# Optimization experiments

Measured on AMD Instinct MI355X. Metric: run time of the kernel, lower is better.

Reference implementation:

```python
import jax, jax.numpy as jnp
import numpy as np

B = 8192
IN = 2048
H = 2048


def setup_inputs() -> dict:
    key = jax.random.key(0)
    ks = jax.random.split(key, 7)
    s_in = 1.0 / np.sqrt(IN)
    s_h = 1.0 / np.sqrt(H)
    inp = jax.random.normal(ks[0], (B, IN), jnp.float32)
    h0 = jax.random.normal(ks[1], (B, H), jnp.float32)
    c0 = jax.random.normal(ks[2], (B, H), jnp.float32)
    # Packed gate weights: columns ordered [i, f, o, g], each block size H.
    # Equivalent to the 8 separate nn.Linear layers (i_w,f_w,o_w,g_w / i_u,f_u,o_u,g_u).
    W = jax.random.uniform(ks[3], (IN, 4 * H), jnp.float32, -s_in, s_in)
    b_w = jax.random.uniform(ks[4], (4 * H,), jnp.float32, -s_in, s_in)
    U = jax.random.uniform(ks[5], (H, 4 * H), jnp.float32, -s_h, s_h)
    b_u = jax.random.uniform(ks[6], (4 * H,), jnp.float32, -s_h, s_h)
    return {"inp": inp, "h0": h0, "c0": c0, "W": W, "b_w": b_w, "U": U, "b_u": b_u}


def reference(inp, h0, c0, W, b_w, U, b_u):
    # Two big GEMMs instead of eight small ones; identical math.
    gates = inp @ W + b_w + h0 @ U + b_u  # [B, 4H]
    i_g, f_g, o_g, g_g = jnp.split(gates, 4, axis=-1)
    i = jax.nn.sigmoid(i_g)
    f = jax.nn.sigmoid(f_g)
    o = jax.nn.sigmoid(o_g)
    g = jnp.tanh(g_g)
    c = f * c0 + i * g
    h = o * jnp.tanh(c)
    return (h, c)
```

## Files before the change

### kernel.cpp

```cpp
#include <hip/hip_runtime.h>
#include <hip/hip_bf16.h>

#define B_DIM 8192
#define IN_DIM 2048
#define H_DIM 2048
#define K_DIM 4096
#define N4H   8192
#define NT    64

using short8 = __attribute__((ext_vector_type(8))) short;
using f32x4  = __attribute__((ext_vector_type(4))) float;
using u16x4  = __attribute__((ext_vector_type(4))) unsigned short;

__device__ __forceinline__ unsigned short f2bf(float f) {
  union { float f; unsigned int u; } v; v.f = f;
  unsigned int u = v.u;
  return (unsigned short)((u + 0x7FFFu + ((u >> 16) & 1u)) >> 16);
}

__global__ __launch_bounds__(256) void pack_a(const float* __restrict__ inp,
                                              const float* __restrict__ h0,
                                              unsigned short* __restrict__ Ap) {
  size_t idx = ((size_t)blockIdx.x * 256 + threadIdx.x) * 4;
  int b = (int)(idx >> 12);
  int k = (int)(idx & 4095);
  const float* src = (k < IN_DIM) ? (inp + (size_t)b * IN_DIM + k)
                                  : (h0  + (size_t)b * H_DIM + (k - IN_DIM));
  float4 v = *(const float4*)src;
  u16x4 o = { f2bf(v.x), f2bf(v.y), f2bf(v.z), f2bf(v.w) };
  *(u16x4*)&Ap[idx] = o;
}

__global__ __launch_bounds__(256) void pack_b(const float* __restrict__ W,
                                              const float* __restrict__ U,
                                              unsigned short* __restrict__ Bp) {
  __shared__ float tile[64][17];
  const int c0 = blockIdx.x * 16;
  const int k0 = blockIdx.y * 64;
  const int gate  = (c0 >> 4) & 3;
  const int jbase = (c0 >> 6) * 16;
  const int colbase = gate * 2048 + jbase;
  const int t  = threadIdx.x;
  const int cc = t & 15;
  const int r0 = t >> 4;
#pragma unroll
  for (int rr = 0; rr < 4; ++rr) {
    int k = k0 + r0 + rr * 16;
    const float* src = (k < IN_DIM) ? (W + (size_t)k * N4H)
                                    : (U + (size_t)(k - IN_DIM) * N4H);
    tile[r0 + rr * 16][cc] = src[colbase + cc];
  }
  __syncthreads();
  const int c   = t >> 4;
  const int kk0 = (t & 15) * 4;
  u16x4 o = { f2bf(tile[kk0 + 0][c]), f2bf(tile[kk0 + 1][c]),
              f2bf(tile[kk0 + 2][c]), f2bf(tile[kk0 + 3][c]) };
  *(u16x4*)&Bp[(size_t)(c0 + c) * K_DIM + k0 + kk0] = o;
}

__global__ __launch_bounds__(512, 2) void lstm_gemm(
    const unsigned short* __restrict__ Ap,
    const unsigned short* __restrict__ Bp,
    const float* __restrict__ c0,
    const float* __restrict__ b_w,
    const float* __restrict__ b_u,
    float* __restrict__ out) {
  __shared__ unsigned short lds[65536];

  const int t     = threadIdx.x;
  const int lane  = t & 63;
  const int wid   = t >> 6;
  const int wr    = wid >> 2;
  const int wc    = wid & 3;
  const int laneM = lane & 15;
  const int laneG = lane >> 4;

  const int wg  = blockIdx.x;
  const int swz = (wg & 7) * 128 + (wg >> 3);
  const int bm  = swz >> 5;
  const int bn  = swz & 31;

  const int rt   = t >> 3;
  const int gt   = t & 7;
  const int gsw  = gt ^ (rt & 7);
  const unsigned short* gA = Ap + (size_t)(bm * 256 + rt) * K_DIM + gsw * 8;
  const unsigned short* gB = Bp + (size_t)(bn * 256 + rt) * K_DIM + gsw * 8;

#define STAGE(gptr, ldsoff)                                                   \
  __builtin_amdgcn_global_load_lds(                                           \
      (const __attribute__((address_space(1))) void*)(gptr),                  \
      (__attribute__((address_space(3))) void*)&lds[(ldsoff) + t * 8], 16, 0, 0)

  const int sbit = laneM & 7;
  int aoff[2], boff[2];
#pragma unroll
  for (int kk = 0; kk < 2; ++kk) {
    aoff[kk] = wr * 8192 + laneM * 64 + ((kk * 4 + laneG) ^ sbit) * 8;
    boff[kk] = 16384 + (wc >> 1) * 8192 + ((wc & 1) * 64 + laneM) * 64
               + ((kk * 4 + laneG) ^ sbit) * 8;
  }

  f32x4 acc[8][4];
#pragma unroll
  for (int m = 0; m < 8; ++m)
#pragma unroll
    for (int n = 0; n < 4; ++n)
      acc[m][n] = (f32x4){0.f, 0.f, 0.f, 0.f};

  short8 bf[4][2];

  STAGE(gB,               16384 + 0);
  STAGE(gB +  64 * K_DIM, 16384 + 4096);
  STAGE(gB + 128 * K_DIM, 16384 + 8192);
  STAGE(gB + 192 * K_DIM, 16384 + 12288);
  STAGE(gA,               0);
  STAGE(gA +  64 * K_DIM, 4096);
  STAGE(gA + 128 * K_DIM, 8192);
  STAGE(gA + 192 * K_DIM, 12288);
  asm volatile("s_waitcnt vmcnt(0)" ::: "memory");
  __builtin_amdgcn_s_barrier();

  for (int kt = 0; kt < NT - 1; ++kt) {
    const int cb = (kt & 1) * 32768;
    const int db = ((kt & 1) ^ 1) * 32768;
    const unsigned short* gA1 = gA + (kt + 1) * 64;
    const unsigned short* gB1 = gB + (kt + 1) * 64;
#pragma unroll
    for (int q = 0; q < 4; ++q) {
      short8 af[2][2];
      if (q == 0) {
#pragma unroll
        for (int n = 0; n < 4; ++n)
#pragma unroll
          for (int kk = 0; kk < 2; ++kk)
            bf[n][kk] = *(const short8*)&lds[cb + boff[kk] + n * 1024];
      }
#pragma unroll
      for (int i = 0; i < 2; ++i)
#pragma unroll
        for (int kk = 0; kk < 2; ++kk)
          af[i][kk] = *(const short8*)&lds[cb + aoff[kk] + (2 * q + i) * 1024];

      if (q == 0) {
        STAGE(gB1,               db + 16384 + 0);
        STAGE(gB1 +  64 * K_DIM, db + 16384 + 4096);
      } else if (q == 1) {
        STAGE(gB1 + 128 * K_DIM, db + 16384 + 8192);
        STAGE(gB1 + 192 * K_DIM, db + 16384 + 12288);
        asm volatile("s_waitcnt vmcnt(4)" ::: "memory");
      } else if (q == 2) {
        STAGE(gA1,               db + 0);
        STAGE(gA1 + 128 * K_DIM, db + 8192);
      } else {
        STAGE(gA1 +  64 * K_DIM, db + 4096);
        STAGE(gA1 + 192 * K_DIM, db + 12288);
        asm volatile("s_waitcnt vmcnt(2)" ::: "memory");
      }
      __builtin_amdgcn_s_barrier();
      __builtin_amdgcn_s_setprio(1);
#pragma unroll
      for (int i = 0; i < 2; ++i)
#pragma unroll
        for (int n = 0; n < 4; ++n)
#pragma unroll
          for (int kk = 0; kk < 2; ++kk)
            acc[2 * q + i][n] = __builtin_amdgcn_mfma_f32_16x16x32_bf16(
                af[i][kk], bf[n][kk], acc[2 * q + i][n], 0, 0, 0);
      __builtin_amdgcn_s_setprio(0);
      __builtin_amdgcn_s_barrier();
    }
  }

  asm volatile("s_waitcnt vmcnt(0)" ::: "memory");
  __builtin_amdgcn_s_barrier();
  {
    const int cb = ((NT - 1) & 1) * 32768;
#pragma unroll
    for (int q = 0; q < 4; ++q) {
      short8 af[2][2];
      if (q == 0) {
#pragma unroll
        for (int n = 0; n < 4; ++n)
#pragma unroll
          for (int kk = 0; kk < 2; ++kk)
            bf[n][kk] = *(const short8*)&lds[cb + boff[kk] + n * 1024];
      }
#pragma unroll
      for (int i = 0; i < 2; ++i)
#pragma unroll
        for (int kk = 0; kk < 2; ++kk)
          af[i][kk] = *(const short8*)&lds[cb + aoff[kk] + (2 * q + i) * 1024];
      __builtin_amdgcn_s_setprio(1);
#pragma unroll
      for (int i = 0; i < 2; ++i)
#pragma unroll
        for (int n = 0; n < 4; ++n)
#pragma unroll
          for (int kk = 0; kk < 2; ++kk)
            acc[2 * q + i][n] = __builtin_amdgcn_mfma_f32_16x16x32_bf16(
                af[i][kk], bf[n][kk], acc[2 * q + i][n], 0, 0, 0);
      __builtin_amdgcn_s_setprio(0);
    }
  }

  const int j = (bn * 4 + wc) * 16 + laneM;
  float bias[4];
#pragma unroll
  for (int g = 0; g < 4; ++g)
    bias[g] = b_w[g * 2048 + j] + b_u[g * 2048 + j];

  const int rbase = bm * 256 + wr * 128 + laneG * 4;
  float* outH = out;
  float* outC = out + (size_t)B_DIM * H_DIM;
#pragma unroll
  for (int m = 0; m < 8; ++m) {
#pragma unroll
    for (int r = 0; r < 4; ++r) {
      const int bi = rbase + m * 16 + r;
      const size_t off = (size_t)bi * H_DIM + j;
      float ig = acc[m][0][r] + bias[0];
      float fg = acc[m][1][r] + bias[1];
      float og = acc[m][2][r] + bias[2];
      float gg = acc[m][3][r] + bias[3];
      float iv = 1.f / (1.f + __expf(-ig));
      float fv = 1.f / (1.f + __expf(-fg));
      float ov = 1.f / (1.f + __expf(-og));
      float gv = 2.f / (1.f + __expf(-2.f * gg)) - 1.f;
      float cv = fv * c0[off] + iv * gv;
      float tc = 2.f / (1.f + __expf(-2.f * cv)) - 1.f;
      outH[off] = ov * tc;
      outC[off] = cv;
    }
  }
}

extern "C" void kernel_launch(void* const* d_in, const int* in_sizes, int n_in,
                              void* d_out, int out_size, void* d_ws, size_t ws_size,
                              hipStream_t stream) {
  const float* inp = (const float*)d_in[0];
  const float* h0  = (const float*)d_in[1];
  const float* c0  = (const float*)d_in[2];
  const float* W   = (const float*)d_in[3];
  const float* b_w = (const float*)d_in[4];
  const float* U   = (const float*)d_in[5];
  const float* b_u = (const float*)d_in[6];
  float* out = (float*)d_out;

  unsigned short* Ap = (unsigned short*)d_ws;
  unsigned short* Bp = Ap + (size_t)B_DIM * K_DIM;

  pack_a<<<(B_DIM * K_DIM / 4) / 256, 256, 0, stream>>>(inp, h0, Ap);
  dim3 gb(N4H / 16, K_DIM / 64);
  pack_b<<<gb, 256, 0, stream>>>(W, U, Bp);
  lstm_gemm<<<1024, 512, 0, stream>>>(Ap, Bp, c0, b_w, b_u, out);
}
```

Before: 659.5 us.

## Software-pipeline LDS fragment reads ahead of MFMAs with finer-grained staging waits

```diff
diff --git a/kernel.cpp b/kernel.cpp
--- a/kernel.cpp
+++ b/kernel.cpp
@@ -91,6 +91,14 @@
       (const __attribute__((address_space(1))) void*)(gptr),                  \
       (__attribute__((address_space(3))) void*)&lds[(ldsoff) + t * 8], 16, 0, 0)
 
+#define VMCNT(n) asm volatile("s_waitcnt vmcnt(" #n ")" ::: "memory")
+#define BARF()                                                                \
+  do {                                                                        \
+    asm volatile("" ::: "memory");                                            \
+    __builtin_amdgcn_s_barrier();                                             \
+    asm volatile("" ::: "memory");                                            \
+  } while (0)
+
   const int sbit = laneM & 7;
   int aoff[2], boff[2];
 #pragma unroll
@@ -100,6 +108,32 @@
                + ((kk * 4 + laneG) ^ sbit) * 8;
   }
 
+#define RD_AF(AF, BASE, PH)                                                   \
+  _Pragma("unroll")                                                           \
+  for (int i = 0; i < 2; ++i)                                                 \
+    _Pragma("unroll")                                                         \
+    for (int kk = 0; kk < 2; ++kk)                                            \
+      AF[i][kk] = *(const short8*)&lds[(BASE) + aoff[kk] + (2 * (PH) + i) * 1024];
+
+#define RD_BF(BASE)                                                           \
+  _Pragma("unroll")                                                           \
+  for (int n = 0; n < 4; ++n)                                                 \
+    _Pragma("unroll")                                                         \
+    for (int kk = 0; kk < 2; ++kk)                                            \
+      bfr[n][kk] = *(const short8*)&lds[(BASE) + boff[kk] + n * 1024];
+
+#define MFMA16(Q, AF)                                                         \
+  __builtin_amdgcn_s_setprio(1);                                              \
+  _Pragma("unroll")                                                           \
+  for (int i = 0; i < 2; ++i)                                                 \
+    _Pragma("unroll")                                                         \
+    for (int n = 0; n < 4; ++n)                                               \
+      _Pragma("unroll")                                                       \
+      for (int kk = 0; kk < 2; ++kk)                                          \
+        acc[2 * (Q) + i][n] = __builtin_amdgcn_mfma_f32_16x16x32_bf16(        \
+            AF[i][kk], bfr[n][kk], acc[2 * (Q) + i][n], 0, 0, 0);             \
+  __builtin_amdgcn_s_setprio(0)
+
   f32x4 acc[8][4];
 #pragma unroll
   for (int m = 0; m < 8; ++m)
@@ -107,107 +141,78 @@
     for (int n = 0; n < 4; ++n)
       acc[m][n] = (f32x4){0.f, 0.f, 0.f, 0.f};
 
-  short8 bf[4][2];
-
-  STAGE(gB,               16384 + 0);
+  short8 af0[2][2], af1[2][2], bfr[4][2];
+
+  const int j = (bn * 4 + wc) * 16 + laneM;
+  float bias[4];
+#pragma unroll
+  for (int g = 0; g < 4; ++g)
+    bias[g] = b_w[g * 2048 + j] + b_u[g * 2048 + j];
+  asm volatile("s_waitcnt vmcnt(0)" ::: "memory");
+
+  STAGE(gA,               0);
+  STAGE(gA + 128 * K_DIM, 8192);
+  STAGE(gB,               16384);
   STAGE(gB +  64 * K_DIM, 16384 + 4096);
   STAGE(gB + 128 * K_DIM, 16384 + 8192);
   STAGE(gB + 192 * K_DIM, 16384 + 12288);
-  STAGE(gA,               0);
   STAGE(gA +  64 * K_DIM, 4096);
-  STAGE(gA + 128 * K_DIM, 8192);
   STAGE(gA + 192 * K_DIM, 12288);
-  asm volatile("s_waitcnt vmcnt(0)" ::: "memory");
-  __builtin_amdgcn_s_barrier();
-
+  VMCNT(4);
+  BARF();
+  RD_AF(af0, 0, 0);
+  if (wc < 2) RD_BF(0);
+
+#pragma unroll 1
   for (int kt = 0; kt < NT - 1; ++kt) {
-    const int cb = (kt & 1) * 32768;
-    const int db = ((kt & 1) ^ 1) * 32768;
+    const int cb = (kt & 1) << 15;
+    const int db = cb ^ 32768;
     const unsigned short* gA1 = gA + (kt + 1) * 64;
     const unsigned short* gB1 = gB + (kt + 1) * 64;
-#pragma unroll
-    for (int q = 0; q < 4; ++q) {
-      short8 af[2][2];
-      if (q == 0) {
-#pragma unroll
-        for (int n = 0; n < 4; ++n)
-#pragma unroll
-          for (int kk = 0; kk < 2; ++kk)
-            bf[n][kk] = *(const short8*)&lds[cb + boff[kk] + n * 1024];
-      }
-#pragma unroll
-      for (int i = 0; i < 2; ++i)
-#pragma unroll
-        for (int kk = 0; kk < 2; ++kk)
-          af[i][kk] = *(const short8*)&lds[cb + aoff[kk] + (2 * q + i) * 1024];
-
-      if (q == 0) {
-        STAGE(gB1,               db + 16384 + 0);
-        STAGE(gB1 +  64 * K_DIM, db + 16384 + 4096);
-      } else if (q == 1) {
-        STAGE(gB1 + 128 * K_DIM, db + 16384 + 8192);
-        STAGE(gB1 + 192 * K_DIM, db + 16384 + 12288);
-        asm volatile("s_waitcnt vmcnt(4)" ::: "memory");
-      } else if (q == 2) {
-        STAGE(gA1,               db + 0);
-        STAGE(gA1 + 128 * K_DIM, db + 8192);
-      } else {
-        STAGE(gA1 +  64 * K_DIM, db + 4096);
-        STAGE(gA1 + 192 * K_DIM, db + 12288);
-        asm volatile("s_waitcnt vmcnt(2)" ::: "memory");
-      }
-      __builtin_amdgcn_s_barrier();
-      __builtin_amdgcn_s_setprio(1);
-#pragma unroll
-      for (int i = 0; i < 2; ++i)
-#pragma unroll
-        for (int n = 0; n < 4; ++n)
-#pragma unroll
-          for (int kk = 0; kk < 2; ++kk)
-            acc[2 * q + i][n] = __builtin_amdgcn_mfma_f32_16x16x32_bf16(
-                af[i][kk], bf[n][kk], acc[2 * q + i][n], 0, 0, 0);
-      __builtin_amdgcn_s_setprio(0);
-      __builtin_amdgcn_s_barrier();
-    }
-  }
-
-  asm volatile("s_waitcnt vmcnt(0)" ::: "memory");
-  __builtin_amdgcn_s_barrier();
+    STAGE(gA1,               db + 0);
+    STAGE(gA1 + 128 * K_DIM, db + 8192);
+    VMCNT(4);
+    BARF();
+    if (wc >= 2) RD_BF(cb);
+    RD_AF(af1, cb, 1);
+    MFMA16(0, af0);
+    STAGE(gB1,               db + 16384);
+    STAGE(gB1 +  64 * K_DIM, db + 16384 + 4096);
+    VMCNT(4);
+    BARF();
+    RD_AF(af0, cb, 2);
+    MFMA16(1, af1);
+    STAGE(gB1 + 128 * K_DIM, db + 16384 + 8192);
+    STAGE(gB1 + 192 * K_DIM, db + 16384 + 12288);
+    BARF();
+    RD_AF(af1, cb, 3);
+    MFMA16(2, af0);
+    STAGE(gA1 +  64 * K_DIM, db + 4096);
+    STAGE(gA1 + 192 * K_DIM, db + 12288);
+    VMCNT(4);
+    BARF();
+    RD_AF(af0, db, 0);
+    MFMA16(3, af1);
+    if (wc < 2) RD_BF(db);
+    BARF();
+  }
+
   {
-    const int cb = ((NT - 1) & 1) * 32768;
-#pragma unroll
-    for (int q = 0; q < 4; ++q) {
-      short8 af[2][2];
-      if (q == 0) {
-#pragma unroll
-        for (int n = 0; n < 4; ++n)
-#pragma unroll
-          for (int kk = 0; kk < 2; ++kk)
-            bf[n][kk] = *(const short8*)&lds[cb + boff[kk] + n * 1024];
-      }
-#pragma unroll
-      for (int i = 0; i < 2; ++i)
-#pragma unroll
-        for (int kk = 0; kk < 2; ++kk)
-          af[i][kk] = *(const short8*)&lds[cb + aoff[kk] + (2 * q + i) * 1024];
-      __builtin_amdgcn_s_setprio(1);
-#pragma unroll
-      for (int i = 0; i < 2; ++i)
-#pragma unroll
-        for (int n = 0; n < 4; ++n)
-#pragma unroll
-          for (int kk = 0; kk < 2; ++kk)
-            acc[2 * q + i][n] = __builtin_amdgcn_mfma_f32_16x16x32_bf16(
-                af[i][kk], bf[n][kk], acc[2 * q + i][n], 0, 0, 0);
-      __builtin_amdgcn_s_setprio(0);
-    }
-  }
-
-  const int j = (bn * 4 + wc) * 16 + laneM;
-  float bias[4];
-#pragma unroll
-  for (int g = 0; g < 4; ++g)
-    bias[g] = b_w[g * 2048 + j] + b_u[g * 2048 + j];
+    VMCNT(2);
+    BARF();
+    if (wc >= 2) RD_BF(32768);
+    RD_AF(af1, 32768, 1);
+    MFMA16(0, af0);
+    VMCNT(0);
+    BARF();
+    RD_AF(af0, 32768, 2);
+    MFMA16(1, af1);
+    BARF();
+    RD_AF(af1, 32768, 3);
+    MFMA16(2, af0);
+    BARF();
+    MFMA16(3, af1);
+  }
 
   const int rbase = bm * 256 + wr * 128 + laneG * 4;
   float* outH = out;
```

New measurement: 574.0 us. -13.0%, faster.
